# Kernel optimization log

Measured on AMD Instinct MI355X. Metric: run time of the kernel, lower is better.

## Reference

```python
import jax, jax.numpy as jnp
import numpy as np

PAD = 1      # init_kwargs: padding
STRIDE = 1   # init_kwargs: stride


def setup_inputs() -> dict:
    key = jax.random.key(0)
    k1, k2 = jax.random.split(key)
    # x: [C=4, H=4096, W=4096] input feature map (no batch dim in original module)
    x = jax.random.normal(k1, (4, 4096, 4096), dtype=jnp.float32)
    # kernel: [cout=4, cin=4, h=3, w=3] learned conv weight (nn.Parameter)
    kernel = jax.random.normal(k2, (4, 4, 3, 3), dtype=jnp.float32)
    return {"x": x, "kernel": kernel}


def reference(x, kernel):
    # Faithful math: zero-pad by PAD on all four spatial sides, then a direct
    # cross-correlation (torch conv semantics) with stride STRIDE.
    # Original loops over output pixels; here it's a single fused conv primitive.
    out = jax.lax.conv_general_dilated(
        x[None],                      # [1, C, H, W]
        kernel,                       # [cout, cin, h, w]
        window_strides=(STRIDE, STRIDE),
        padding=[(PAD, PAD), (PAD, PAD)],
        dimension_numbers=("NCHW", "OIHW", "NCHW"),
    )
    return out[0]                     # [cout, hout, wout]
```

## Files before the change

### kernel.cpp

```cpp
#include <hip/hip_runtime.h>


#define IW 4096
#define IH 4096
constexpr long long HWsz = (long long)IH * IW;

typedef float v4f __attribute__((ext_vector_type(4)));

__device__ __forceinline__ void gload_lds16(const float* g, float* l) {
    __builtin_amdgcn_global_load_lds(
        (const __attribute__((address_space(1))) char*)g,
        (__attribute__((address_space(3))) char*)l, 16, 0, 0);
}

__device__ __forceinline__ void stage(const float* __restrict__ xin, int ci,
                                      float (*rbuf)[512], int y0, int X0,
                                      int w, int l) {
    const float* plane = xin + (long long)ci * HWsz;
    #pragma unroll
    for (int k = 0; k < 5; ++k) {
        const int c = 5 * w + k;
        const int r = c >> 1;
        const int h = c & 1;
        int yy = y0 - 1 + r;
        int yc = yy < 0 ? 0 : (yy >= IH ? IH - 1 : yy);
        gload_lds16(plane + (long long)yc * IW + (X0 + 256 * h + 4 * l),
                    &rbuf[r][256 * h]);
    }
}

__device__ __forceinline__ void compute_ci(float acc[4][4][4],
                                           const float (*rbuf)[512],
                                           const float hl[6], const float hr[6],
                                           const float* __restrict__ wt,
                                           int ci, int y0, int p_u, int tx) {
    #pragma unroll
    for (int dy = 0; dy < 6; ++dy) {
        const int r  = 4 * p_u + dy;
        const int yy = y0 - 1 + r;
        if (yy >= 0 && yy < IH) {
            const v4f a = *reinterpret_cast<const v4f*>(&rbuf[r][4 * tx]);
            const float L = (tx == 0)   ? hl[dy] : rbuf[r][4 * tx - 1];
            const float R = (tx == 127) ? hr[dy] : rbuf[r][4 * tx + 4];
            float vv[6] = {L, a.x, a.y, a.z, a.w, R};
            #pragma unroll
            for (int rk = 0; rk < 3; ++rk) {
                const int o = dy - rk;
                if (o >= 0 && o < 4) {
                    #pragma unroll
                    for (int co = 0; co < 4; ++co) {
                        #pragma unroll
                        for (int kx = 0; kx < 3; ++kx) {
                            const float w = wt[((co * 4 + ci) * 3 + rk) * 3 + kx];
                            #pragma unroll
                            for (int p = 0; p < 4; ++p)
                                acc[o][co][p] = fmaf(w, vv[p + kx], acc[o][co][p]);
                        }
                    }
                }
            }
        }
    }
}

__global__ __launch_bounds__(256) void conv3x3_kernel(
    const float* __restrict__ xin,
    const float* __restrict__ wt,
    float* __restrict__ out)
{
    __shared__ __align__(16) float rows[2][10][512];

    const int bid = blockIdx.x;
    const int swz = (bid & 7) * 512 + (bid >> 3);
    const int rowblk = swz >> 3;
    const int xs     = swz & 7;
    const int y0     = rowblk << 3;
    const int X0     = xs << 9;
    const int t      = (int)threadIdx.x;
    const int w      = t >> 6, l = t & 63;
    const int tx     = t & 127;
    const int p_u    = __builtin_amdgcn_readfirstlane(t >> 7);

    float hl[4][6], hr[4][6];
    #pragma unroll
    for (int ci = 0; ci < 4; ++ci) {
        const float* plane = xin + (long long)ci * HWsz;
        #pragma unroll
        for (int dy = 0; dy < 6; ++dy) {
            const int yy = y0 - 1 + 4 * p_u + dy;
            const bool vrow = (yy >= 0 && yy < IH);
            const long long rb = (long long)(vrow ? yy : 0) * IW;
            hl[ci][dy] = (vrow && X0 > 0)        ? plane[rb + X0 - 1]   : 0.f;
            hr[ci][dy] = (vrow && X0 + 512 < IW) ? plane[rb + X0 + 512] : 0.f;
        }
    }

    float acc[4][4][4];
    #pragma unroll
    for (int o = 0; o < 4; ++o)
        #pragma unroll
        for (int co = 0; co < 4; ++co)
            #pragma unroll
            for (int p = 0; p < 4; ++p) acc[o][co][p] = 0.f;

    stage(xin, 0, rows[0], y0, X0, w, l);

    stage(xin, 1, rows[1], y0, X0, w, l);
    asm volatile("s_waitcnt vmcnt(5)\n\ts_barrier" ::: "memory");
    compute_ci(acc, rows[0], hl[0], hr[0], wt, 0, y0, p_u, tx);
    asm volatile("s_barrier" ::: "memory");
    stage(xin, 2, rows[0], y0, X0, w, l);
    asm volatile("s_waitcnt vmcnt(5)\n\ts_barrier" ::: "memory");
    compute_ci(acc, rows[1], hl[1], hr[1], wt, 1, y0, p_u, tx);
    asm volatile("s_barrier" ::: "memory");
    stage(xin, 3, rows[1], y0, X0, w, l);
    asm volatile("s_waitcnt vmcnt(5)\n\ts_barrier" ::: "memory");
    compute_ci(acc, rows[0], hl[2], hr[2], wt, 2, y0, p_u, tx);
    asm volatile("s_barrier" ::: "memory");
    asm volatile("s_waitcnt vmcnt(0)\n\ts_barrier" ::: "memory");
    compute_ci(acc, rows[1], hl[3], hr[3], wt, 3, y0, p_u, tx);

    const int x0g = X0 + 4 * tx;
    #pragma unroll
    for (int o = 0; o < 4; ++o) {
        const long long obase = (long long)(y0 + 4 * p_u + o) * IW + x0g;
        #pragma unroll
        for (int co = 0; co < 4; ++co) {
            v4f ov;
            ov.x = acc[o][co][0]; ov.y = acc[o][co][1];
            ov.z = acc[o][co][2]; ov.w = acc[o][co][3];
            __builtin_nontemporal_store(ov,
                reinterpret_cast<v4f*>(out + co * HWsz + obase));
        }
    }
}

extern "C" void kernel_launch(void* const* d_in, const int* in_sizes, int n_in,
                              void* d_out, int out_size, void* d_ws, size_t ws_size,
                              hipStream_t stream) {
    const float* xin = (const float*)d_in[0];
    const float* wt  = (const float*)d_in[1];
    float* out       = (float*)d_out;

    dim3 grid(4096), block(256);
    hipLaunchKernelGGL(conv3x3_kernel, grid, block, 0, stream, xin, wt, out);
}
```

Measured before the change: 90.52 us.

## Halve block tile width to 256 columns and assign two output rows per wave

Each block now covers an 8x256 output tile instead of 8x512, so the grid doubles and LDS use per block halves. Each wave computes 2 output rows of 256 pixels instead of 4 rows of 4 pixels for half the block, and the staging loads are redistributed unevenly across waves (3,3,2,2 rows) with per-wave waitcnt values. This aims for more resident blocks and lower register pressure, at the cost of more halo overhead: each wave reads 4 input rows to produce 2 output rows, and the column halo is twice as frequent.

Measured after the change: 90.89 us. No clear change (+0.4%).

```diff
diff --git a/kernel.cpp b/kernel.cpp
--- a/kernel.cpp
+++ b/kernel.cpp
@@ -14,39 +14,40 @@
 }
 
 __device__ __forceinline__ void stage(const float* __restrict__ xin, int ci,
-                                      float (*rbuf)[512], int y0, int X0,
-                                      int w, int l) {
+                                      float (*rbuf)[256], int y0, int X0,
+                                      int w_u, int nw, int base, int l) {
     const float* plane = xin + (long long)ci * HWsz;
     #pragma unroll
-    for (int k = 0; k < 5; ++k) {
-        const int c = 5 * w + k;
-        const int r = c >> 1;
-        const int h = c & 1;
-        int yy = y0 - 1 + r;
-        int yc = yy < 0 ? 0 : (yy >= IH ? IH - 1 : yy);
-        gload_lds16(plane + (long long)yc * IW + (X0 + 256 * h + 4 * l),
-                    &rbuf[r][256 * h]);
+    for (int k = 0; k < 3; ++k) {
+        if (k < nw) {
+            const int r = base + k;
+            int yy = y0 - 1 + r;
+            int yc = yy < 0 ? 0 : (yy >= IH ? IH - 1 : yy);
+            gload_lds16(plane + (long long)yc * IW + (X0 + 4 * l),
+                        &rbuf[r][0]);
+        }
     }
 }
 
-__device__ __forceinline__ void compute_ci(float acc[4][4][4],
-                                           const float (*rbuf)[512],
-                                           const float hl[6], const float hr[6],
+__device__ __forceinline__ void compute_ci(float acc[2][4][4],
+                                           const float (*rbuf)[256],
+                                           const float hl[4], const float hr[4],
                                            const float* __restrict__ wt,
-                                           int ci, int y0, int p_u, int tx) {
+                                           int ci, int y0, int w_u,
+                                           int l, int iL, int iR) {
     #pragma unroll
-    for (int dy = 0; dy < 6; ++dy) {
-        const int r  = 4 * p_u + dy;
+    for (int dy = 0; dy < 4; ++dy) {
+        const int r  = 2 * w_u + dy;
         const int yy = y0 - 1 + r;
         if (yy >= 0 && yy < IH) {
-            const v4f a = *reinterpret_cast<const v4f*>(&rbuf[r][4 * tx]);
-            const float L = (tx == 0)   ? hl[dy] : rbuf[r][4 * tx - 1];
-            const float R = (tx == 127) ? hr[dy] : rbuf[r][4 * tx + 4];
+            const v4f a = *reinterpret_cast<const v4f*>(&rbuf[r][4 * l]);
+            const float L = (l == 0)  ? hl[dy] : rbuf[r][iL];
+            const float R = (l == 63) ? hr[dy] : rbuf[r][iR];
             float vv[6] = {L, a.x, a.y, a.z, a.w, R};
             #pragma unroll
             for (int rk = 0; rk < 3; ++rk) {
                 const int o = dy - rk;
-                if (o >= 0 && o < 4) {
+                if (o >= 0 && o < 2) {
                     #pragma unroll
                     for (int co = 0; co < 4; ++co) {
                         #pragma unroll
@@ -68,62 +69,74 @@
     const float* __restrict__ wt,
     float* __restrict__ out)
 {
-    __shared__ __align__(16) float rows[2][10][512];
+    __shared__ __align__(16) float rows[2][10][256];
 
     const int bid = blockIdx.x;
-    const int swz = (bid & 7) * 512 + (bid >> 3);
-    const int rowblk = swz >> 3;
-    const int xs     = swz & 7;
+    const int swz = (bid & 7) * 1024 + (bid >> 3);
+    const int rowblk = swz >> 4;
+    const int xs     = swz & 15;
     const int y0     = rowblk << 3;
-    const int X0     = xs << 9;
+    const int X0     = xs << 8;
     const int t      = (int)threadIdx.x;
-    const int w      = t >> 6, l = t & 63;
-    const int tx     = t & 127;
-    const int p_u    = __builtin_amdgcn_readfirstlane(t >> 7);
+    const int l      = t & 63;
+    const int w_u    = __builtin_amdgcn_readfirstlane(t >> 6);
+    const int yw     = y0 + 2 * w_u;
+    const bool xlo   = (X0 == 0);
+    const bool xhi   = (X0 + 256 == IW);
+    const int iL = (l == 0)  ? 0   : 4 * l - 1;
+    const int iR = (l == 63) ? 0   : 4 * l + 4;
+    const int nw   = (w_u < 2) ? 3 : 2;
+    const int base = (w_u < 2) ? 3 * w_u : 6 + 2 * (w_u - 2);
 
-    float hl[4][6], hr[4][6];
+    float hl[4][4], hr[4][4];
     #pragma unroll
     for (int ci = 0; ci < 4; ++ci) {
         const float* plane = xin + (long long)ci * HWsz;
         #pragma unroll
-        for (int dy = 0; dy < 6; ++dy) {
-            const int yy = y0 - 1 + 4 * p_u + dy;
+        for (int dy = 0; dy < 4; ++dy) {
+            const int yy = yw - 1 + dy;
             const bool vrow = (yy >= 0 && yy < IH);
             const long long rb = (long long)(vrow ? yy : 0) * IW;
-            hl[ci][dy] = (vrow && X0 > 0)        ? plane[rb + X0 - 1]   : 0.f;
-            hr[ci][dy] = (vrow && X0 + 512 < IW) ? plane[rb + X0 + 512] : 0.f;
+            hl[ci][dy] = (vrow && !xlo) ? plane[rb + X0 - 1]   : 0.f;
+            hr[ci][dy] = (vrow && !xhi) ? plane[rb + X0 + 256] : 0.f;
         }
     }
 
-    float acc[4][4][4];
+    float acc[2][4][4];
     #pragma unroll
-    for (int o = 0; o < 4; ++o)
+    for (int o = 0; o < 2; ++o)
         #pragma unroll
         for (int co = 0; co < 4; ++co)
             #pragma unroll
             for (int p = 0; p < 4; ++p) acc[o][co][p] = 0.f;
 
-    stage(xin, 0, rows[0], y0, X0, w, l);
+    stage(xin, 0, rows[0], y0, X0, w_u, nw, base, l);
 
-    stage(xin, 1, rows[1], y0, X0, w, l);
-    asm volatile("s_waitcnt vmcnt(5)\n\ts_barrier" ::: "memory");
-    compute_ci(acc, rows[0], hl[0], hr[0], wt, 0, y0, p_u, tx);
+    stage(xin, 1, rows[1], y0, X0, w_u, nw, base, l);
+    if (w_u < 2) asm volatile("s_waitcnt vmcnt(3)" ::: "memory");
+    else         asm volatile("s_waitcnt vmcnt(2)" ::: "memory");
     asm volatile("s_barrier" ::: "memory");
-    stage(xin, 2, rows[0], y0, X0, w, l);
-    asm volatile("s_waitcnt vmcnt(5)\n\ts_barrier" ::: "memory");
-    compute_ci(acc, rows[1], hl[1], hr[1], wt, 1, y0, p_u, tx);
+    compute_ci(acc, rows[0], hl[0], hr[0], wt, 0, y0, w_u, l, iL, iR);
     asm volatile("s_barrier" ::: "memory");
-    stage(xin, 3, rows[1], y0, X0, w, l);
-    asm volatile("s_waitcnt vmcnt(5)\n\ts_barrier" ::: "memory");
-    compute_ci(acc, rows[0], hl[2], hr[2], wt, 2, y0, p_u, tx);
+    stage(xin, 2, rows[0], y0, X0, w_u, nw, base, l);
+    if (w_u < 2) asm volatile("s_waitcnt vmcnt(3)" ::: "memory");
+    else         asm volatile("s_waitcnt vmcnt(2)" ::: "memory");
+    asm volatile("s_barrier" ::: "memory");
+    compute_ci(acc, rows[1], hl[1], hr[1], wt, 1, y0, w_u, l, iL, iR);
+    asm volatile("s_barrier" ::: "memory");
+    stage(xin, 3, rows[1], y0, X0, w_u, nw, base, l);
+    if (w_u < 2) asm volatile("s_waitcnt vmcnt(3)" ::: "memory");
+    else         asm volatile("s_waitcnt vmcnt(2)" ::: "memory");
+    asm volatile("s_barrier" ::: "memory");
+    compute_ci(acc, rows[0], hl[2], hr[2], wt, 2, y0, w_u, l, iL, iR);
     asm volatile("s_barrier" ::: "memory");
     asm volatile("s_waitcnt vmcnt(0)\n\ts_barrier" ::: "memory");
-    compute_ci(acc, rows[1], hl[3], hr[3], wt, 3, y0, p_u, tx);
+    compute_ci(acc, rows[1], hl[3], hr[3], wt, 3, y0, w_u, l, iL, iR);
 
-    const int x0g = X0 + 4 * tx;
+    const int x0g = X0 + 4 * l;
     #pragma unroll
-    for (int o = 0; o < 4; ++o) {
-        const long long obase = (long long)(y0 + 4 * p_u + o) * IW + x0g;
+    for (int o = 0; o < 2; ++o) {
+        const long long obase = (long long)(yw + o) * IW + x0g;
         #pragma unroll
         for (int co = 0; co < 4; ++co) {
             v4f ov;
@@ -142,6 +155,6 @@
     const float* wt  = (const float*)d_in[1];
     float* out       = (float*)d_out;
 
-    dim3 grid(4096), block(256);
+    dim3 grid(8192), block(256);
     hipLaunchKernelGGL(conv3x3_kernel, grid, block, 0, stream, xin, wt, out);
 }
```

## Halve rows per block and use triple-buffered LDS staging with doubled grid

Applied to the files above, without the earlier changes.

Each block now computes 4 output rows instead of 8, so each thread accumulates 2 output rows instead of 4. The grid doubles to 8192 blocks and the block-index swizzle is adjusted to match. The LDS buffer changes from two 10-row buffers to three 6-row buffers, so three input channels are prefetched ahead with adjusted waitcnt values. The aim is lower register and LDS use per block, hence more resident waves and better latency hiding, at the cost of more redundant halo-row loads relative to useful rows.

Result: faster. 87.49 us (-3.4%).

```diff
diff --git a/kernel.cpp b/kernel.cpp
--- a/kernel.cpp
+++ b/kernel.cpp
@@ -18,8 +18,8 @@
                                       int w, int l) {
     const float* plane = xin + (long long)ci * HWsz;
     #pragma unroll
-    for (int k = 0; k < 5; ++k) {
-        const int c = 5 * w + k;
+    for (int k = 0; k < 3; ++k) {
+        const int c = 3 * w + k;
         const int r = c >> 1;
         const int h = c & 1;
         int yy = y0 - 1 + r;
@@ -29,24 +29,25 @@
     }
 }
 
-__device__ __forceinline__ void compute_ci(float acc[4][4][4],
+__device__ __forceinline__ void compute_ci(float acc[2][4][4],
                                            const float (*rbuf)[512],
-                                           const float hl[6], const float hr[6],
+                                           const float hl[4], const float hr[4],
                                            const float* __restrict__ wt,
-                                           int ci, int y0, int p_u, int tx) {
+                                           int ci, int y0, int p_u,
+                                           int txs, int iL, int iR) {
     #pragma unroll
-    for (int dy = 0; dy < 6; ++dy) {
-        const int r  = 4 * p_u + dy;
+    for (int dy = 0; dy < 4; ++dy) {
+        const int r  = 2 * p_u + dy;
         const int yy = y0 - 1 + r;
         if (yy >= 0 && yy < IH) {
-            const v4f a = *reinterpret_cast<const v4f*>(&rbuf[r][4 * tx]);
-            const float L = (tx == 0)   ? hl[dy] : rbuf[r][4 * tx - 1];
-            const float R = (tx == 127) ? hr[dy] : rbuf[r][4 * tx + 4];
+            const v4f a = *reinterpret_cast<const v4f*>(&rbuf[r][4 * txs]);
+            const float L = (txs == 0)   ? hl[dy] : rbuf[r][iL];
+            const float R = (txs == 127) ? hr[dy] : rbuf[r][iR];
             float vv[6] = {L, a.x, a.y, a.z, a.w, R};
             #pragma unroll
             for (int rk = 0; rk < 3; ++rk) {
                 const int o = dy - rk;
-                if (o >= 0 && o < 4) {
+                if (o >= 0 && o < 2) {
                     #pragma unroll
                     for (int co = 0; co < 4; ++co) {
                         #pragma unroll
@@ -68,26 +69,29 @@
     const float* __restrict__ wt,
     float* __restrict__ out)
 {
-    __shared__ __align__(16) float rows[2][10][512];
+    __shared__ __align__(16) float rows[3][6][512];
 
     const int bid = blockIdx.x;
-    const int swz = (bid & 7) * 512 + (bid >> 3);
+    const int swz = (bid & 7) * 1024 + (bid >> 3);
     const int rowblk = swz >> 3;
     const int xs     = swz & 7;
-    const int y0     = rowblk << 3;
+    const int y0     = rowblk << 2;
     const int X0     = xs << 9;
     const int t      = (int)threadIdx.x;
     const int w      = t >> 6, l = t & 63;
-    const int tx     = t & 127;
+    const int txs    = t & 127;
     const int p_u    = __builtin_amdgcn_readfirstlane(t >> 7);
+    const int yw     = y0 + 2 * p_u;
+    const int iL = (txs == 0)   ? 0 : 4 * txs - 1;
+    const int iR = (txs == 127) ? 0 : 4 * txs + 4;
 
-    float hl[4][6], hr[4][6];
+    float hl[4][4], hr[4][4];
     #pragma unroll
     for (int ci = 0; ci < 4; ++ci) {
         const float* plane = xin + (long long)ci * HWsz;
         #pragma unroll
-        for (int dy = 0; dy < 6; ++dy) {
-            const int yy = y0 - 1 + 4 * p_u + dy;
+        for (int dy = 0; dy < 4; ++dy) {
+            const int yy = yw - 1 + dy;
             const bool vrow = (yy >= 0 && yy < IH);
             const long long rb = (long long)(vrow ? yy : 0) * IW;
             hl[ci][dy] = (vrow && X0 > 0)        ? plane[rb + X0 - 1]   : 0.f;
@@ -95,35 +99,33 @@
         }
     }
 
-    float acc[4][4][4];
+    float acc[2][4][4];
     #pragma unroll
-    for (int o = 0; o < 4; ++o)
+    for (int o = 0; o < 2; ++o)
         #pragma unroll
         for (int co = 0; co < 4; ++co)
             #pragma unroll
             for (int p = 0; p < 4; ++p) acc[o][co][p] = 0.f;
 
     stage(xin, 0, rows[0], y0, X0, w, l);
+    stage(xin, 1, rows[1], y0, X0, w, l);
 
-    stage(xin, 1, rows[1], y0, X0, w, l);
-    asm volatile("s_waitcnt vmcnt(5)\n\ts_barrier" ::: "memory");
-    compute_ci(acc, rows[0], hl[0], hr[0], wt, 0, y0, p_u, tx);
+    stage(xin, 2, rows[2], y0, X0, w, l);
+    asm volatile("s_waitcnt vmcnt(6)\n\ts_barrier" ::: "memory");
+    compute_ci(acc, rows[0], hl[0], hr[0], wt, 0, y0, p_u, txs, iL, iR);
     asm volatile("s_barrier" ::: "memory");
-    stage(xin, 2, rows[0], y0, X0, w, l);
-    asm volatile("s_waitcnt vmcnt(5)\n\ts_barrier" ::: "memory");
-    compute_ci(acc, rows[1], hl[1], hr[1], wt, 1, y0, p_u, tx);
-    asm volatile("s_barrier" ::: "memory");
-    stage(xin, 3, rows[1], y0, X0, w, l);
-    asm volatile("s_waitcnt vmcnt(5)\n\ts_barrier" ::: "memory");
-    compute_ci(acc, rows[0], hl[2], hr[2], wt, 2, y0, p_u, tx);
-    asm volatile("s_barrier" ::: "memory");
+    stage(xin, 3, rows[0], y0, X0, w, l);
+    asm volatile("s_waitcnt vmcnt(6)\n\ts_barrier" ::: "memory");
+    compute_ci(acc, rows[1], hl[1], hr[1], wt, 1, y0, p_u, txs, iL, iR);
+    asm volatile("s_waitcnt vmcnt(3)\n\ts_barrier" ::: "memory");
+    compute_ci(acc, rows[2], hl[2], hr[2], wt, 2, y0, p_u, txs, iL, iR);
     asm volatile("s_waitcnt vmcnt(0)\n\ts_barrier" ::: "memory");
-    compute_ci(acc, rows[1], hl[3], hr[3], wt, 3, y0, p_u, tx);
+    compute_ci(acc, rows[0], hl[3], hr[3], wt, 3, y0, p_u, txs, iL, iR);
 
-    const int x0g = X0 + 4 * tx;
+    const int x0g = X0 + 4 * txs;
     #pragma unroll
-    for (int o = 0; o < 4; ++o) {
-        const long long obase = (long long)(y0 + 4 * p_u + o) * IW + x0g;
+    for (int o = 0; o < 2; ++o) {
+        const long long obase = (long long)(yw + o) * IW + x0g;
         #pragma unroll
         for (int co = 0; co < 4; ++co) {
             v4f ov;
@@ -142,6 +144,6 @@
     const float* wt  = (const float*)d_in[1];
     float* out       = (float*)d_out;
 
-    dim3 grid(4096), block(256);
+    dim3 grid(8192), block(256);
     hipLaunchKernelGGL(conv3x3_kernel, grid, block, 0, stream, xin, wt, out);
 }
```
